# Performance work log

Hardware: AMD Instinct MI355X
Metric: run time of the kernel (lower is better)

## Reference

```python
import jax, jax.numpy as jnp
import numpy as np

NUM_EXPERTS = 8
TOP_K = 2
BALANCE_LOSS_COEF = 0.01


def setup_inputs() -> dict:
    key = jax.random.key(0)
    ks = jax.random.split(key, 5)
    B, S, H, I, E = 8, 2048, 512, 2048, NUM_EXPERTS
    return {
        "hidden_states": jax.random.normal(ks[0], (B, S, H), dtype=jnp.float32),
        "Wg": jax.random.normal(ks[1], (H, E), dtype=jnp.float32) * (1.0 / np.sqrt(H)),
        "bg": jnp.zeros((E,), dtype=jnp.float32),
        "W1": jax.random.normal(ks[2], (E, H, I), dtype=jnp.float32) * (1.0 / np.sqrt(H)),
        "b1": jnp.zeros((E, I), dtype=jnp.float32),
        "W2": jax.random.normal(ks[3], (E, I, H), dtype=jnp.float32) * (1.0 / np.sqrt(I)),
        "b2": jnp.zeros((E, H), dtype=jnp.float32),
    }


def reference(hidden_states, Wg, bg, W1, b1, W2, b2):
    B, S, H = hidden_states.shape
    E, K = NUM_EXPERTS, TOP_K

    # ---- Router: softmax gate + top-k, renormalized weights ----
    logits = jnp.einsum('bsh,he->bse', hidden_states, Wg) + bg       # [B,S,E]
    probs = jax.nn.softmax(logits, axis=-1)                          # [B,S,E]
    top_p, top_i = jax.lax.top_k(probs, K)                           # [B,S,K]
    routing_weights = top_p / jnp.sum(top_p, axis=-1, keepdims=True)  # [B,S,K]

    # ---- Experts: compute every expert densely (small fixed E), then gather ----
    h = jnp.einsum('bsh,ehi->ebsi', hidden_states, W1) + b1[:, None, None, :]
    h = jax.nn.gelu(h)
    y = jnp.einsum('ebsi,eih->ebsh', h, W2) + b2[:, None, None, :]   # [E,B,S,H]

    y = jnp.moveaxis(y, 0, 2)                                        # [B,S,E,H]
    sel = jnp.take_along_axis(y, top_i[..., None], axis=2)           # [B,S,K,H]
    output = jnp.sum(routing_weights[..., None] * sel, axis=2) + hidden_states

    # ---- Load balancing loss (Switch-style): E * sum_e f_e * P_e ----
    assign = jnp.sum(jax.nn.one_hot(top_i, E, dtype=probs.dtype), axis=2)  # [B,S,E]
    f = jnp.mean(assign, axis=(0, 1)) / K                            # fraction dispatched
    P = jnp.mean(probs, axis=(0, 1))                                 # mean router prob
    balance_loss = BALANCE_LOSS_COEF * E * jnp.sum(f * P)

    return output, balance_loss
```

## Files before the change

### kernel.cpp

```cpp
#include <hip/hip_runtime.h>

#define BS_TOK 16384
#define HD 512
#define IDIM 2048
#define NE 8
#define RT_MAX 264
#define CAP (RT_MAX * 128)

typedef unsigned short u16;
typedef unsigned int u32;
typedef __attribute__((ext_vector_type(8))) __bf16 bf16x8;
typedef __attribute__((ext_vector_type(4))) float f32x4;

__device__ __forceinline__ u16 f2bf(float f) {
  u32 u = __builtin_bit_cast(u32, f);
  u += 0x7fffu + ((u >> 16) & 1u);
  return (u16)(u >> 16);
}
__device__ __forceinline__ float bflo(u32 u) { return __builtin_bit_cast(float, u << 16); }
__device__ __forceinline__ float bfhi(u32 u) { return __builtin_bit_cast(float, u & 0xffff0000u); }
__device__ __forceinline__ float gelu_t(float v) {
  float c = 0.7978845608028654f * (v + 0.044715f * v * v * v);
  return v / (1.0f + __expf(-2.0f * c));
}
__device__ __forceinline__ void gload16(const u16* g, u16* l) {
  __builtin_amdgcn_global_load_lds((const __attribute__((address_space(1))) u16*)g,
                                   (__attribute__((address_space(3))) u16*)l, 16, 0, 0);
}

__global__ void k_init(u32* counts, u32* pos, float* Psum, int* perm_t, float* perm_w) {
  int i = blockIdx.x * 256 + threadIdx.x;
  if (i < NE) { counts[i] = 0; pos[i] = 0; Psum[i] = 0.f; }
  if (i < CAP) { perm_t[i] = 0; perm_w[i] = 0.f; }
}

__global__ void k_transpose2(const float* __restrict__ W1, u16* __restrict__ W1T,
                             const float* __restrict__ W2, u16* __restrict__ W2T) {
  __shared__ float t[32][33];
  int z = blockIdx.z;
  const float* in; u16* out; int R, C, bx, by;
  if (z < NE) { in = W1; out = W1T; R = HD; C = IDIM; bx = blockIdx.x; by = blockIdx.y; }
  else { in = W2; out = W2T; R = IDIM; C = HD; bx = blockIdx.y; by = blockIdx.x; z -= NE; }
  size_t eb = (size_t)z * HD * IDIM;
  int c0 = bx * 32, r0 = by * 32;
  int tx = threadIdx.x, ty = threadIdx.y;
  #pragma unroll
  for (int j = ty; j < 32; j += 8) t[j][tx] = in[eb + (size_t)(r0 + j) * C + (c0 + tx)];
  __syncthreads();
  #pragma unroll
  for (int j = ty; j < 32; j += 8) out[eb + (size_t)(c0 + j) * R + (r0 + tx)] = f2bf(t[tx][j]);
}

__global__ void k_router(const float* __restrict__ x, const float* __restrict__ Wg,
                         const float* __restrict__ bg, int* __restrict__ top_e,
                         float* __restrict__ top_w, u32* __restrict__ counts,
                         float* __restrict__ Psum, u16* __restrict__ xb) {
  __shared__ float wg_s[HD * NE];
  __shared__ float Pp[NE];
  __shared__ u32 cnt[NE];
  int tid = threadIdx.x;
  if (tid < NE) { Pp[tid] = 0.f; cnt[tid] = 0; }
  for (int i = tid; i < HD * NE; i += 256) wg_s[i] = Wg[i];
  __syncthreads();
  int wv = tid >> 6, lane = tid & 63;
  int t = blockIdx.x * 4 + wv;
  const float4* xr = (const float4*)(x + (size_t)t * HD + lane * 8);
  float4 a = xr[0], b = xr[1];
  u32 p0 = f2bf(a.x) | ((u32)f2bf(a.y) << 16);
  u32 p1 = f2bf(a.z) | ((u32)f2bf(a.w) << 16);
  u32 p2 = f2bf(b.x) | ((u32)f2bf(b.y) << 16);
  u32 p3 = f2bf(b.z) | ((u32)f2bf(b.w) << 16);
  ((uint4*)(xb + (size_t)t * HD))[lane] = make_uint4(p0, p1, p2, p3);

  float acc[NE];
  #pragma unroll
  for (int e = 0; e < NE; ++e) acc[e] = 0.f;
  #pragma unroll
  for (int j = 0; j < 8; ++j) {
    float xv = j < 4 ? (&a.x)[j] : (&b.x)[j - 4];
    int h = lane * 8 + j;
    #pragma unroll
    for (int e = 0; e < NE; ++e) acc[e] += xv * wg_s[h * NE + e];
  }
  #pragma unroll
  for (int off = 32; off > 0; off >>= 1) {
    #pragma unroll
    for (int e = 0; e < NE; ++e) acc[e] += __shfl_down(acc[e], off);
  }
  if (lane == 0) {
    float lg[NE];
    #pragma unroll
    for (int e = 0; e < NE; ++e) lg[e] = acc[e] + bg[e];
    int i1 = 0; float m1 = lg[0];
    #pragma unroll
    for (int e = 1; e < NE; ++e) if (lg[e] > m1) { m1 = lg[e]; i1 = e; }
    int i2 = -1; float m2 = -1e30f;
    #pragma unroll
    for (int e = 0; e < NE; ++e) if (e != i1 && lg[e] > m2) { m2 = lg[e]; i2 = e; }
    float s = 0.f, p[NE];
    #pragma unroll
    for (int e = 0; e < NE; ++e) { p[e] = __expf(lg[e] - m1); s += p[e]; }
    float inv = 1.f / s;
    #pragma unroll
    for (int e = 0; e < NE; ++e) { p[e] *= inv; atomicAdd(&Pp[e], p[e]); }
    float denom = p[i1] + p[i2];
    top_e[2 * t] = i1; top_e[2 * t + 1] = i2;
    top_w[2 * t] = p[i1] / denom; top_w[2 * t + 1] = p[i2] / denom;
    atomicAdd(&cnt[i1], 1u); atomicAdd(&cnt[i2], 1u);
  }
  __syncthreads();
  if (tid < NE) { atomicAdd(&counts[tid], cnt[tid]); atomicAdd(&Psum[tid], Pp[tid]); }
}

__global__ void k_scan(const u32* __restrict__ counts, const float* __restrict__ Psum,
                       u32* __restrict__ padoff, u32* __restrict__ pos, float* __restrict__ out) {
  if (threadIdx.x == 0) {
    u32 off = 0; float loss = 0.f;
    for (int e = 0; e < NE; ++e) {
      padoff[e] = off; pos[e] = off;
      off += ((counts[e] + 127u) / 128u) * 128u;
      loss += ((float)counts[e] / (float)(BS_TOK * 2)) * (Psum[e] / (float)BS_TOK);
    }
    padoff[NE] = off;
    out[(size_t)BS_TOK * HD] = 0.01f * (float)NE * loss;
  }
}

__global__ void k_scatter(const int* __restrict__ top_e, const float* __restrict__ top_w,
                          u32* __restrict__ pos, int* __restrict__ perm_t,
                          float* __restrict__ perm_w, int* __restrict__ inv) {
  int g = blockIdx.x * 256 + threadIdx.x;
  int e = top_e[g]; float wgt = top_w[g];
  int lane = threadIdx.x & 63;
  #pragma unroll
  for (int ee = 0; ee < NE; ++ee) {
    unsigned long long m = __ballot(e == ee);
    if (e == ee) {
      int nb = __popcll(m & ((1ull << lane) - 1ull));
      int leader = __ffsll((unsigned long long)m) - 1;
      u32 base = 0;
      if (lane == leader) base = atomicAdd(&pos[ee], (u32)__popcll(m));
      base = __shfl(base, leader);
      int slot = (int)base + nb;
      perm_t[slot] = g >> 1;
      perm_w[slot] = wgt;
      inv[g] = slot;
    }
  }
}

__global__ void k_outinit(const float* __restrict__ x, float* __restrict__ out) {
  size_t i = (size_t)blockIdx.x * 256 + threadIdx.x;
  ((float4*)out)[i] = ((const float4*)x)[i];
}

template <int KSTEPS, int NCT, int NTOT, bool GATHER, bool ACT, bool ATOMIC>
__global__ __launch_bounds__(256, 2) void k_gemm(
    const u16* __restrict__ A, int lda, const u16* __restrict__ W,
    const float* __restrict__ bias, const int* __restrict__ perm_t,
    const float* __restrict__ perm_w, const u32* __restrict__ padoff,
    u16* __restrict__ C, float* __restrict__ outA, int rt0) {
  __shared__ u16 As[2][8192], Bs[2][8192];
  int nb = gridDim.x;
  int b = blockIdx.x;
  int tile = (b & 7) * (nb >> 3) + (b >> 3);
  int rt = rt0 + tile / NCT, ct = tile % NCT;
  u32 s0 = (u32)rt * 128u;
  if (rt >= RT_MAX || s0 >= padoff[NE]) return;
  int e = 0;
  #pragma unroll
  for (int k = 1; k < NE; ++k) e += (s0 >= padoff[k]) ? 1 : 0;

  int tid = threadIdx.x;
  int wv = tid >> 6, lane = tid & 63;
  int l15 = lane & 15, lg4 = lane >> 4;
  int wr = wv >> 1, wc = wv & 1;

  int srow = tid >> 3;
  int cb = (tid & 7) * 16;
  int cbs = (cb ^ ((srow & 7) << 4)) >> 1;

  const u16* ap[4]; const u16* bp[4];
  #pragma unroll
  for (int i = 0; i < 4; ++i) {
    int r = i * 32 + srow;
    int arow = GATHER ? perm_t[s0 + r] : (int)(s0 + r);
    ap[i] = A + (size_t)arow * lda + cbs;
    bp[i] = W + ((size_t)e * NTOT + ct * 128 + r) * (KSTEPS * 64) + cbs;
  }

  f32x4 acc[4][4] = {};

  #pragma unroll
  for (int i = 0; i < 4; ++i) gload16(ap[i], As[0] + tid * 8 + i * 2048);
  #pragma unroll
  for (int i = 0; i < 4; ++i) gload16(bp[i], Bs[0] + tid * 8 + i * 2048);
  __syncthreads();

  for (int ks = 0; ks < KSTEPS; ++ks) {
    int cur = ks & 1;
    if (ks + 1 < KSTEPS) {
      int k0 = (ks + 1) * 64;
      #pragma unroll
      for (int i = 0; i < 4; ++i) gload16(ap[i] + k0, As[cur ^ 1] + tid * 8 + i * 2048);
      #pragma unroll
      for (int i = 0; i < 4; ++i) gload16(bp[i] + k0, Bs[cur ^ 1] + tid * 8 + i * 2048);
    }
    const u16* Ab = As[cur];
    const u16* Bb = Bs[cur];
    #pragma unroll
    for (int kk = 0; kk < 2; ++kk) {
      bf16x8 af[4], bf[4];
      #pragma unroll
      for (int f = 0; f < 4; ++f) {
        int ra = wr * 64 + f * 16 + l15;
        af[f] = *(const bf16x8*)((const char*)Ab +
                 (ra * 128 + ((kk * 64 + lg4 * 16) ^ ((ra & 7) << 4))));
        int rb = wc * 64 + f * 16 + l15;
        bf[f] = *(const bf16x8*)((const char*)Bb +
                 (rb * 128 + ((kk * 64 + lg4 * 16) ^ ((rb & 7) << 4))));
      }
      #pragma unroll
      for (int i = 0; i < 4; ++i)
        #pragma unroll
        for (int j = 0; j < 4; ++j)
          acc[i][j] = __builtin_amdgcn_mfma_f32_16x16x32_bf16(af[i], bf[j], acc[i][j], 0, 0, 0);
    }
    __syncthreads();
  }

  int base_n = ct * 128 + wc * 64;
  float bv[4];
  #pragma unroll
  for (int j = 0; j < 4; ++j) bv[j] = bias[e * NTOT + base_n + j * 16 + l15];

  #pragma unroll
  for (int i = 0; i < 4; ++i) {
    u32 mrow = s0 + wr * 64 + i * 16 + lg4 * 4;
    #pragma unroll
    for (int rr = 0; rr < 4; ++rr) {
      u32 m = mrow + rr;
      if (ATOMIC) {
        int tok = perm_t[m]; float wt = perm_w[m];
        if (wt != 0.f) {
          #pragma unroll
          for (int j = 0; j < 4; ++j) {
            float v = (acc[i][j][rr] + bv[j]) * wt;
            atomicAdd(outA + (size_t)tok * HD + base_n + j * 16 + l15, v);
          }
        }
      } else {
        #pragma unroll
        for (int j = 0; j < 4; ++j) {
          float v = acc[i][j][rr] + bv[j];
          if (ACT) v = gelu_t(v);
          C[(size_t)m * NTOT + base_n + j * 16 + l15] = f2bf(v);
        }
      }
    }
  }
}

__global__ void k_final(const float* __restrict__ x, const u16* __restrict__ y,
                        const int* __restrict__ inv, const float* __restrict__ top_w,
                        float* __restrict__ out) {
  int tid = threadIdx.x;
  int t = blockIdx.x * 4 + (tid >> 6);
  int lane = tid & 63;
  int s0 = inv[2 * t], s1 = inv[2 * t + 1];
  float w0 = top_w[2 * t], w1 = top_w[2 * t + 1];
  size_t xo = (size_t)t * HD + lane * 8;
  float4 a = *(const float4*)(x + xo);
  float4 b = *(const float4*)(x + xo + 4);
  uint4 ya = *(const uint4*)(y + (size_t)s0 * HD + lane * 8);
  uint4 yb = *(const uint4*)(y + (size_t)s1 * HD + lane * 8);
  float4 o0, o1;
  o0.x = a.x + w0 * bflo(ya.x) + w1 * bflo(yb.x);
  o0.y = a.y + w0 * bfhi(ya.x) + w1 * bfhi(yb.x);
  o0.z = a.z + w0 * bflo(ya.y) + w1 * bflo(yb.y);
  o0.w = a.w + w0 * bfhi(ya.y) + w1 * bfhi(yb.y);
  o1.x = b.x + w0 * bflo(ya.z) + w1 * bflo(yb.z);
  o1.y = b.y + w0 * bfhi(ya.z) + w1 * bfhi(yb.z);
  o1.z = b.z + w0 * bflo(ya.w) + w1 * bflo(yb.w);
  o1.w = b.w + w0 * bfhi(ya.w) + w1 * bfhi(yb.w);
  *(float4*)(out + xo) = o0;
  *(float4*)(out + xo + 4) = o1;
}

extern "C" void kernel_launch(void* const* d_in, const int* in_sizes, int n_in,
                              void* d_out, int out_size, void* d_ws, size_t ws_size,
                              hipStream_t stream) {
  const float* x  = (const float*)d_in[0];
  const float* Wg = (const float*)d_in[1];
  const float* bg = (const float*)d_in[2];
  const float* W1 = (const float*)d_in[3];
  const float* b1 = (const float*)d_in[4];
  const float* W2 = (const float*)d_in[5];
  const float* b2 = (const float*)d_in[6];
  float* out = (float*)d_out;

  char* w = (char*)d_ws;
  u32* counts  = (u32*)(w + 0);
  u32* pos     = (u32*)(w + 32);
  float* Psum  = (float*)(w + 64);
  u32* padoff  = (u32*)(w + 96);
  int* top_e   = (int*)(w + 256);
  float* top_w = (float*)(w + 256 + 131072);
  int* invm    = (int*)(w + 256 + 2 * 131072);
  int* perm_t  = (int*)(w + 256 + 3 * 131072);
  float* perm_w = (float*)(w + 256 + 3 * 131072 + 135168);
  u16* xb  = (u16*)(w + 663808);
  u16* W1T = (u16*)(w + 17441024);
  u16* W2T = (u16*)(w + 34218240);
  u16* h   = (u16*)(w + 50995456);
  u16* y   = (u16*)(w + 189407488);

  bool modeA = ws_size >= 224010496ull;
  int T;
  if (modeA) {
    T = RT_MAX;
  } else {
    size_t hspace = ws_size > 50995456ull ? ws_size - 50995456ull : 0;
    T = (int)(hspace / (128ull * IDIM * 2));
    T &= ~1;
    if (T < 2) return;
    if (T > RT_MAX) T = RT_MAX;
  }

  k_init<<<(CAP + 255) / 256, 256, 0, stream>>>(counts, pos, Psum, perm_t, perm_w);
  k_transpose2<<<dim3(IDIM / 32, HD / 32, 2 * NE), dim3(32, 8), 0, stream>>>(W1, W1T, W2, W2T);
  k_router<<<BS_TOK / 4, 256, 0, stream>>>(x, Wg, bg, top_e, top_w, counts, Psum, xb);
  k_scan<<<1, 64, 0, stream>>>(counts, Psum, padoff, pos, out);
  k_scatter<<<(BS_TOK * 2) / 256, 256, 0, stream>>>(top_e, top_w, pos, perm_t, perm_w, invm);
  if (!modeA) k_outinit<<<(BS_TOK * HD / 4) / 256, 256, 0, stream>>>(x, out);

  int nch = (RT_MAX + T - 1) / T;
  for (int c = 0; c < nch; ++c) {
    int rt0 = c * T;
    u16* hadj = h - (size_t)rt0 * 128 * IDIM;
    k_gemm<8, 16, IDIM, true, true, false><<<T * 16, 256, 0, stream>>>(
        xb, HD, W1T, b1, perm_t, perm_w, padoff, hadj, nullptr, rt0);
    if (modeA) {
      k_gemm<32, 4, HD, false, false, false><<<T * 4, 256, 0, stream>>>(
          hadj, IDIM, W2T, b2, perm_t, perm_w, padoff, y, nullptr, rt0);
    } else {
      k_gemm<32, 4, HD, false, false, true><<<T * 4, 256, 0, stream>>>(
          hadj, IDIM, W2T, b2, perm_t, perm_w, padoff, nullptr, out, rt0);
    }
  }
  if (modeA) k_final<<<BS_TOK / 4, 256, 0, stream>>>(x, y, invm, top_w, out);
}
```

Before: 418.6 us.

## Deepen GEMM prefetch to two stages with register-staged fragments and fine waitcnts

The GEMM main loop now issues global-to-LDS loads two K-steps ahead instead of one. Each step reads all LDS fragments into registers, then barriers, so the just-consumed buffer can be refilled while MFMAs run. Full __syncthreads are replaced by explicit vmcnt/lgkmcnt waits, raw s_barrier, and s_setprio around the MFMA block. The aim is to hide more global-load latency and reduce barrier stalls, at the cost of doubled fragment registers and fragile hand-tuned wait counts.

```diff
diff --git a/kernel.cpp b/kernel.cpp
--- a/kernel.cpp
+++ b/kernel.cpp
@@ -195,38 +195,63 @@
   for (int i = 0; i < 4; ++i) gload16(ap[i], As[0] + tid * 8 + i * 2048);
   #pragma unroll
   for (int i = 0; i < 4; ++i) gload16(bp[i], Bs[0] + tid * 8 + i * 2048);
-  __syncthreads();
+  #pragma unroll
+  for (int i = 0; i < 4; ++i) gload16(ap[i] + 64, As[1] + tid * 8 + i * 2048);
+  #pragma unroll
+  for (int i = 0; i < 4; ++i) gload16(bp[i] + 64, Bs[1] + tid * 8 + i * 2048);
+  asm volatile("s_waitcnt vmcnt(8)" ::: "memory");
+  __builtin_amdgcn_sched_barrier(0);
+  __builtin_amdgcn_s_barrier();
 
   for (int ks = 0; ks < KSTEPS; ++ks) {
     int cur = ks & 1;
-    if (ks + 1 < KSTEPS) {
-      int k0 = (ks + 1) * 64;
-      #pragma unroll
-      for (int i = 0; i < 4; ++i) gload16(ap[i] + k0, As[cur ^ 1] + tid * 8 + i * 2048);
-      #pragma unroll
-      for (int i = 0; i < 4; ++i) gload16(bp[i] + k0, Bs[cur ^ 1] + tid * 8 + i * 2048);
-    }
     const u16* Ab = As[cur];
     const u16* Bb = Bs[cur];
+    bf16x8 af[2][4], bf[2][4];
     #pragma unroll
     for (int kk = 0; kk < 2; ++kk) {
-      bf16x8 af[4], bf[4];
       #pragma unroll
       for (int f = 0; f < 4; ++f) {
         int ra = wr * 64 + f * 16 + l15;
-        af[f] = *(const bf16x8*)((const char*)Ab +
-                 (ra * 128 + ((kk * 64 + lg4 * 16) ^ ((ra & 7) << 4))));
+        af[kk][f] = *(const bf16x8*)((const char*)Ab +
+                    (ra * 128 + ((kk * 64 + lg4 * 16) ^ ((ra & 7) << 4))));
         int rb = wc * 64 + f * 16 + l15;
-        bf[f] = *(const bf16x8*)((const char*)Bb +
-                 (rb * 128 + ((kk * 64 + lg4 * 16) ^ ((rb & 7) << 4))));
+        bf[kk][f] = *(const bf16x8*)((const char*)Bb +
+                    (rb * 128 + ((kk * 64 + lg4 * 16) ^ ((rb & 7) << 4))));
       }
+    }
+    asm volatile("s_waitcnt lgkmcnt(0)" ::: "memory");
+    __builtin_amdgcn_sched_barrier(0);
+    __builtin_amdgcn_s_barrier();
+
+    if (ks + 2 < KSTEPS) {
+      int k0 = (ks + 2) * 64;
+      #pragma unroll
+      for (int i = 0; i < 4; ++i) gload16(ap[i] + k0, As[cur] + tid * 8 + i * 2048);
+      #pragma unroll
+      for (int i = 0; i < 4; ++i) gload16(bp[i] + k0, Bs[cur] + tid * 8 + i * 2048);
+    }
+
+    __builtin_amdgcn_s_setprio(1);
+    #pragma unroll
+    for (int kk = 0; kk < 2; ++kk) {
       #pragma unroll
       for (int i = 0; i < 4; ++i)
         #pragma unroll
         for (int j = 0; j < 4; ++j)
-          acc[i][j] = __builtin_amdgcn_mfma_f32_16x16x32_bf16(af[i], bf[j], acc[i][j], 0, 0, 0);
-    }
-    __syncthreads();
+          acc[i][j] = __builtin_amdgcn_mfma_f32_16x16x32_bf16(af[kk][i], bf[kk][j], acc[i][j], 0, 0, 0);
+    }
+    __builtin_amdgcn_s_setprio(0);
+
+    if (ks + 1 < KSTEPS) {
+      if (ks + 2 < KSTEPS) {
+        asm volatile("s_waitcnt vmcnt(8)" ::: "memory");
+      } else {
+        asm volatile("s_waitcnt vmcnt(0)" ::: "memory");
+      }
+      __builtin_amdgcn_sched_barrier(0);
+      __builtin_amdgcn_s_barrier();
+    }
   }
 
   int base_n = ct * 128 + wc * 64;
```

Result: faster. 380.2 us (-9.2%).
